# Kernel optimization log

Measured on AMD Instinct MI355X. Metric: run time of the kernel, lower is better.

## Reference

```python
import jax, jax.numpy as jnp
import numpy as np

TILE = 8

def _dct_mat():
    # D[k, n] = cos(pi/N * (n + 0.5) * k), matches gen_filters(8,8,dct_coeff)
    k = np.arange(TILE)[:, None]
    n = np.arange(TILE)[None, :]
    return jnp.asarray(np.cos(np.pi / TILE * (n + 0.5) * k), dtype=jnp.float32)

def _idct_mat():
    # ID[k, n] = ((n==0)*(-1/2) + cos(pi/N*(k+0.5)*n)) * sqrt(1/(2N))
    k = np.arange(TILE)[:, None]
    n = np.arange(TILE)[None, :]
    m = ((n == 0) * (-0.5) + np.cos(np.pi / TILE * (k + 0.5) * n)) * np.sqrt(1.0 / (2.0 * TILE))
    return jnp.asarray(m, dtype=jnp.float32)

def _zigzag_tile(keep_count):
    mask = np.zeros((TILE, TILE), dtype=np.float32)
    order = sorted(((x, y) for x in range(TILE) for y in range(TILE)),
                   key=lambda p: (p[0] + p[1], -p[1] if (p[0] + p[1]) % 2 else p[1]))
    for i, j in order[:keep_count]:
        mask[i, j] = 1.0
    return mask

def _yuv_mask(H, W, keeps=(25, 9, 9)):
    chans = []
    for kc in keeps:
        t = _zigzag_tile(kc)
        full = np.tile(t, (int(np.ceil(H / TILE)), int(np.ceil(W / TILE))))[:H, :W]
        chans.append(full)
    return jnp.asarray(np.stack(chans, axis=0), dtype=jnp.float32)  # [3,H,W]

# rgb2yuv / yuv2rgb matrices from the source
_RGB2YUV = jnp.asarray([[0.299, 0.587, 0.114],
                        [-0.14713, -0.28886, 0.436],
                        [0.615, -0.51499, -0.10001]], dtype=jnp.float32)
_YUV2RGB = jnp.asarray([[1.0, 0.0, 1.13983],
                        [1.0, -0.39465, -0.5806],
                        [1.0, 2.03211, 0.0]], dtype=jnp.float32)

def _block_transform(x, M):
    # x: [B,C,H,W]; per non-overlapping 8x8 tile: out = M @ tile @ M^T
    B, C, H, W = x.shape
    xb = x.reshape(B, C, H // TILE, TILE, W // TILE, TILE)
    yb = jnp.einsum('kn,lm,bcinjm->bcikjl', M, M, xb)
    return yb.reshape(B, C, H, W)

def setup_inputs() -> dict:
    key = jax.random.key(0)
    steg = jax.random.normal(key, (16, 3, 512, 512), dtype=jnp.float32)
    return {"steg": steg}

def reference(steg) -> jnp.ndarray:
    B, C, H, W = steg.shape
    pad_h = (TILE - H % TILE) % TILE
    pad_w = (TILE - W % TILE) % TILE
    x = jnp.pad(steg, ((0, 0), (0, 0), (0, pad_h), (0, pad_w)))
    Hp, Wp = H + pad_h, W + pad_w
    # colorspace convert: [B,3,H,W]
    yuv = jnp.einsum('oc,bchw->bohw', _RGB2YUV, x)
    # blockwise DCT, zigzag mask, blockwise IDCT
    dct = _block_transform(yuv, _dct_mat())
    mask = _yuv_mask(Hp, Wp)  # [3,Hp,Wp]
    dct_masked = dct * mask[None]
    idct = _block_transform(dct_masked, _idct_mat())
    rgb = jnp.einsum('oc,bchw->bohw', _YUV2RGB, idct)
    return rgb[:, :, :H, :W]
```

## Files before the change

kernel.cpp:

```cpp
#include <hip/hip_runtime.h>
#include <cstdint>
#include <cstddef>

namespace {

constexpr int TIL = 8;
constexpr int WID = 512;
constexpr int HEI = 512;
constexpr int NB  = 16;
constexpr int TPR = WID / TIL;
constexpr int LSTRIDE = 66;
constexpr int CH = TPR * LSTRIDE;

typedef float vf4 __attribute__((ext_vector_type(4)));

constexpr float C16[17] = {
  1.0f, 0.9807852804032304f, 0.9238795325112867f, 0.8314696123025452f,
  0.7071067811865476f, 0.5555702330196022f, 0.3826834323650898f,
  0.1950903220161283f, 0.0f, -0.1950903220161283f, -0.3826834323650898f,
  -0.5555702330196022f, -0.7071067811865476f, -0.8314696123025452f,
  -0.9238795325112867f, -0.9807852804032304f, -1.0f
};

constexpr float cosp(int t) {
  int a = ((t % 32) + 32) % 32;
  return (a <= 16) ? C16[a] : C16[32 - a];
}

struct Tbl { float D[8][8]; float ID[8][8]; };

constexpr Tbl make_tbl() {
  Tbl t{};
  for (int k = 0; k < 8; ++k)
    for (int n = 0; n < 8; ++n) {
      t.D[k][n] = cosp((2 * n + 1) * k);
      float v = cosp((2 * k + 1) * n);
      if (n == 0) v -= 0.5f;
      t.ID[k][n] = v * 0.25f;
    }
  return t;
}

constexpr Tbl TBL = make_tbl();

constexpr bool keptY(int k, int l) { return (k + l <= 5) || (k + l == 6 && l <= 3); }
constexpr bool keptC(int k, int l) { return (k + l <= 2) || (k + l == 3 && k <= 2); }

template <bool ISY>
__device__ __forceinline__ void tile_transform(float* __restrict__ t) {
  constexpr int KM = ISY ? 7 : 3;

  float T[KM][8];
#pragma unroll
  for (int k = 0; k < KM; ++k)
#pragma unroll
    for (int m = 0; m < 8; ++m) T[k][m] = 0.0f;

#pragma unroll
  for (int n = 0; n < 8; ++n) {
    float x[8];
#pragma unroll
    for (int h = 0; h < 4; ++h) {
      const float2 v = ((const float2*)(t + n * 8))[h];
      x[2 * h] = v.x; x[2 * h + 1] = v.y;
    }
#pragma unroll
    for (int k = 0; k < KM; ++k) {
      const float d = TBL.D[k][n];
#pragma unroll
      for (int m = 0; m < 8; ++m) T[k][m] = __builtin_fmaf(d, x[m], T[k][m]);
    }
  }

  float Uv[KM][8];
#pragma unroll
  for (int k = 0; k < KM; ++k) {
    float yv[8];
#pragma unroll
    for (int l = 0; l < 8; ++l) {
      if (ISY ? keptY(k, l) : keptC(k, l)) {
        float s = 0.0f;
#pragma unroll
        for (int m = 0; m < 8; ++m) s = __builtin_fmaf(T[k][m], TBL.D[l][m], s);
        yv[l] = s;
      }
    }
#pragma unroll
    for (int q = 0; q < 8; ++q) {
      float s = 0.0f;
#pragma unroll
      for (int l = 0; l < 8; ++l)
        if (ISY ? keptY(k, l) : keptC(k, l))
          s = __builtin_fmaf(yv[l], TBL.ID[q][l], s);
      Uv[k][q] = s;
    }
  }

#pragma unroll
  for (int p = 0; p < 8; ++p) {
    float o[8];
#pragma unroll
    for (int q = 0; q < 8; ++q) {
      float s = 0.0f;
#pragma unroll
      for (int k = 0; k < KM; ++k) s = __builtin_fmaf(TBL.ID[p][k], Uv[k][q], s);
      o[q] = s;
    }
#pragma unroll
    for (int h = 0; h < 4; ++h)
      ((float2*)(t + p * 8))[h] = make_float2(o[2 * h], o[2 * h + 1]);
  }
}

__global__ __launch_bounds__(256) void jpeg_kernel(const float* __restrict__ in,
                                                   float* __restrict__ out) {
  __shared__ float lds[3 * CH];
  const int tid = threadIdx.x;
  const int blk = blockIdx.x;
  const int b  = blk >> 6;
  const int ti = blk & 63;
  const size_t plane = (size_t)HEI * WID;
  const size_t base0 = (size_t)b * 3 * plane + (size_t)(ti * TIL) * WID;

  float4 rq[4], gq[4], bq[4];
  int offv[4];
#pragma unroll
  for (int it = 0; it < 4; ++it) {
    const int p4  = it * 256 + tid;
    const int row = p4 >> 7;
    const int col = (p4 & 127) << 2;
    const size_t g = base0 + (size_t)row * WID + col;
    rq[it] = *(const float4*)(in + g);
    gq[it] = *(const float4*)(in + g + plane);
    bq[it] = *(const float4*)(in + g + 2 * plane);
    offv[it] = (col >> 3) * LSTRIDE + row * 8 + (col & 7);
  }
#pragma unroll
  for (int it = 0; it < 4; ++it) {
    const float rr[4] = {rq[it].x, rq[it].y, rq[it].z, rq[it].w};
    const float gg[4] = {gq[it].x, gq[it].y, gq[it].z, gq[it].w};
    const float bb[4] = {bq[it].x, bq[it].y, bq[it].z, bq[it].w};
    float y[4], u[4], v[4];
#pragma unroll
    for (int j = 0; j < 4; ++j) {
      const float R = rr[j], G = gg[j], Bv = bb[j];
      y[j] =  0.299f   * R + 0.587f   * G + 0.114f   * Bv;
      u[j] = -0.14713f * R - 0.28886f * G + 0.436f   * Bv;
      v[j] =  0.615f   * R - 0.51499f * G - 0.10001f * Bv;
    }
    const int off = offv[it];
    ((float2*)(lds + off))[0]          = make_float2(y[0], y[1]);
    ((float2*)(lds + off))[1]          = make_float2(y[2], y[3]);
    ((float2*)(lds + CH + off))[0]     = make_float2(u[0], u[1]);
    ((float2*)(lds + CH + off))[1]     = make_float2(u[2], u[3]);
    ((float2*)(lds + 2 * CH + off))[0] = make_float2(v[0], v[1]);
    ((float2*)(lds + 2 * CH + off))[1] = make_float2(v[2], v[3]);
  }
  __syncthreads();

  if (tid < 192) {
    const int c = tid >> 6;
    float* tp = lds + c * CH + (tid & 63) * LSTRIDE;
    if (c == 0) tile_transform<true>(tp);
    else        tile_transform<false>(tp);
  }
  __syncthreads();

#pragma unroll
  for (int it = 0; it < 4; ++it) {
    const int p4  = it * 256 + tid;
    const int row = p4 >> 7;
    const int col = (p4 & 127) << 2;
    const int off = (col >> 3) * LSTRIDE + row * 8 + (col & 7);
    vf4 ro, go, bo;
#pragma unroll
    for (int h = 0; h < 2; ++h) {
      const float2 yy = ((const float2*)(lds + off))[h];
      const float2 uu = ((const float2*)(lds + CH + off))[h];
      const float2 vv = ((const float2*)(lds + 2 * CH + off))[h];
      ro[2 * h]     = yy.x + 1.13983f * vv.x;
      ro[2 * h + 1] = yy.y + 1.13983f * vv.y;
      go[2 * h]     = yy.x - 0.39465f * uu.x - 0.5806f * vv.x;
      go[2 * h + 1] = yy.y - 0.39465f * uu.y - 0.5806f * vv.y;
      bo[2 * h]     = yy.x + 2.03211f * uu.x;
      bo[2 * h + 1] = yy.y + 2.03211f * uu.y;
    }
    const size_t g = base0 + (size_t)row * WID + col;
    __builtin_nontemporal_store(ro, (vf4*)(out + g));
    __builtin_nontemporal_store(go, (vf4*)(out + g + plane));
    __builtin_nontemporal_store(bo, (vf4*)(out + g + 2 * plane));
  }
}

}

extern "C" void kernel_launch(void* const* d_in, const int* in_sizes, int n_in,
                              void* d_out, int out_size, void* d_ws, size_t ws_size,
                              hipStream_t stream) {
  const float* in = (const float*)d_in[0];
  float* out = (float*)d_out;
  jpeg_kernel<<<dim3(NB * (HEI / TIL)), dim3(256), 0, stream>>>(in, out);
}
```

Measured before the change: 96.92 us.

## Split each tile row across two blocks and assign channels to whole wavefronts

Each block now handles half of an 8-row strip (256 columns), so the grid doubles, the LDS footprint per block halves, and more blocks can be resident at once. The transform phase is remapped so each 32-thread group handles one channel: Y in lanes 0-31, U and V in lanes 64-127. This way the Y and chroma template instantiations no longer share a wavefront. The tradeoff is that 32-63 idle during the transform and each block now does less work relative to its launch and sync overhead.

```diff
diff --git a/kernel.cpp b/kernel.cpp
--- a/kernel.cpp
+++ b/kernel.cpp
@@ -8,9 +8,10 @@
 constexpr int WID = 512;
 constexpr int HEI = 512;
 constexpr int NB  = 16;
-constexpr int TPR = WID / TIL;
+constexpr int HWP = 256;
+constexpr int TPH = HWP / TIL;
 constexpr int LSTRIDE = 66;
-constexpr int CH = TPR * LSTRIDE;
+constexpr int CHP = TPH * LSTRIDE + 8;
 
 typedef float vf4 __attribute__((ext_vector_type(4)));
 
@@ -114,21 +115,23 @@
 
 __global__ __launch_bounds__(256) void jpeg_kernel(const float* __restrict__ in,
                                                    float* __restrict__ out) {
-  __shared__ float lds[3 * CH];
+  __shared__ float lds[3 * CHP];
   const int tid = threadIdx.x;
   const int blk = blockIdx.x;
-  const int b  = blk >> 6;
-  const int ti = blk & 63;
+  const int b  = blk >> 7;
+  const int s  = (blk >> 1) & 63;
+  const int hf = blk & 1;
   const size_t plane = (size_t)HEI * WID;
-  const size_t base0 = (size_t)b * 3 * plane + (size_t)(ti * TIL) * WID;
-
-  float4 rq[4], gq[4], bq[4];
-  int offv[4];
-#pragma unroll
-  for (int it = 0; it < 4; ++it) {
+  const size_t base0 = (size_t)b * 3 * plane + (size_t)(s * TIL) * WID
+                     + (size_t)hf * HWP;
+
+  float4 rq[2], gq[2], bq[2];
+  int offv[2];
+#pragma unroll
+  for (int it = 0; it < 2; ++it) {
     const int p4  = it * 256 + tid;
-    const int row = p4 >> 7;
-    const int col = (p4 & 127) << 2;
+    const int row = p4 >> 6;
+    const int col = (p4 & 63) << 2;
     const size_t g = base0 + (size_t)row * WID + col;
     rq[it] = *(const float4*)(in + g);
     gq[it] = *(const float4*)(in + g + plane);
@@ -136,7 +139,7 @@
     offv[it] = (col >> 3) * LSTRIDE + row * 8 + (col & 7);
   }
 #pragma unroll
-  for (int it = 0; it < 4; ++it) {
+  for (int it = 0; it < 2; ++it) {
     const float rr[4] = {rq[it].x, rq[it].y, rq[it].z, rq[it].w};
     const float gg[4] = {gq[it].x, gq[it].y, gq[it].z, gq[it].w};
     const float bb[4] = {bq[it].x, bq[it].y, bq[it].z, bq[it].w};
@@ -149,35 +152,37 @@
       v[j] =  0.615f   * R - 0.51499f * G - 0.10001f * Bv;
     }
     const int off = offv[it];
-    ((float2*)(lds + off))[0]          = make_float2(y[0], y[1]);
-    ((float2*)(lds + off))[1]          = make_float2(y[2], y[3]);
-    ((float2*)(lds + CH + off))[0]     = make_float2(u[0], u[1]);
-    ((float2*)(lds + CH + off))[1]     = make_float2(u[2], u[3]);
-    ((float2*)(lds + 2 * CH + off))[0] = make_float2(v[0], v[1]);
-    ((float2*)(lds + 2 * CH + off))[1] = make_float2(v[2], v[3]);
+    ((float2*)(lds + off))[0]           = make_float2(y[0], y[1]);
+    ((float2*)(lds + off))[1]           = make_float2(y[2], y[3]);
+    ((float2*)(lds + CHP + off))[0]     = make_float2(u[0], u[1]);
+    ((float2*)(lds + CHP + off))[1]     = make_float2(u[2], u[3]);
+    ((float2*)(lds + 2 * CHP + off))[0] = make_float2(v[0], v[1]);
+    ((float2*)(lds + 2 * CHP + off))[1] = make_float2(v[2], v[3]);
   }
   __syncthreads();
 
-  if (tid < 192) {
-    const int c = tid >> 6;
-    float* tp = lds + c * CH + (tid & 63) * LSTRIDE;
-    if (c == 0) tile_transform<true>(tp);
-    else        tile_transform<false>(tp);
+  if (tid < 128) {
+    if (tid < 32) {
+      tile_transform<true>(lds + tid * LSTRIDE);
+    } else if (tid >= 64) {
+      const int c = (tid >> 5) - 1;
+      tile_transform<false>(lds + c * CHP + (tid & 31) * LSTRIDE);
+    }
   }
   __syncthreads();
 
 #pragma unroll
-  for (int it = 0; it < 4; ++it) {
+  for (int it = 0; it < 2; ++it) {
     const int p4  = it * 256 + tid;
-    const int row = p4 >> 7;
-    const int col = (p4 & 127) << 2;
+    const int row = p4 >> 6;
+    const int col = (p4 & 63) << 2;
     const int off = (col >> 3) * LSTRIDE + row * 8 + (col & 7);
     vf4 ro, go, bo;
 #pragma unroll
     for (int h = 0; h < 2; ++h) {
       const float2 yy = ((const float2*)(lds + off))[h];
-      const float2 uu = ((const float2*)(lds + CH + off))[h];
-      const float2 vv = ((const float2*)(lds + 2 * CH + off))[h];
+      const float2 uu = ((const float2*)(lds + CHP + off))[h];
+      const float2 vv = ((const float2*)(lds + 2 * CHP + off))[h];
       ro[2 * h]     = yy.x + 1.13983f * vv.x;
       ro[2 * h + 1] = yy.y + 1.13983f * vv.y;
       go[2 * h]     = yy.x - 0.39465f * uu.x - 0.5806f * vv.x;
@@ -199,5 +204,5 @@
                               hipStream_t stream) {
   const float* in = (const float*)d_in[0];
   float* out = (float*)d_out;
-  jpeg_kernel<<<dim3(NB * (HEI / TIL)), dim3(256), 0, stream>>>(in, out);
-}
+  jpeg_kernel<<<dim3(NB * (HEI / TIL) * 2), dim3(256), 0, stream>>>(in, out);
+}
```

Result: no change. 98.55 us (+1.7%).
